# Kernel optimization log

Hardware: AMD Instinct MI355X
Metric: run time of the kernel (lower is better)

## Reference

```python
import jax, jax.numpy as jnp
import numpy as np

DIM = 16      # must equal K*K per the module's reshape structure
K = 4         # kernel_size
HEADS = 8
SCALE = (DIM // HEADS) ** (-0.5)


def setup_inputs() -> dict:
    key = jax.random.key(0)
    k1, k2 = jax.random.split(key)
    x = jax.random.normal(k1, (2, 64, 67, 67), dtype=jnp.float32)
    # torch Linear(dim, 3*dim, bias=False) weight: [3*dim, dim]
    w_qkv = jax.random.normal(k2, (3 * DIM, DIM), dtype=jnp.float32) * 0.1
    return {"x": x, "w_qkv": w_qkv}


def reference(x, w_qkv):
    B, C, H, W = x.shape
    k = K
    Ho, Wo = H - k + 1, W - k + 1          # unfold output grid (stride=1)
    L = Ho * Wo
    # Unfold: patches[b, c, i*k+j, ph, pw] = x[b, c, ph+i, pw+j]
    # (matches torch F.unfold channel ordering c-major, then i, then j)
    patches = jnp.stack(
        [x[:, :, i:i + Ho, j:j + Wo] for i in range(k) for j in range(k)],
        axis=2,
    )  # [B, C, k*k, Ho, Wo]
    seq = L // (k * k)                      # L must be divisible by k*k
    # [B*C*k*k, seq, k*k] -- flatten (Ho,Wo)->L row-major then split into (seq, k*k)
    xu = patches.reshape(B * C * k * k, seq, k * k)
    # tiny attention over each row; feature dim = k*k = DIM
    qkv = xu @ w_qkv.T                      # [N, seq, 3*DIM]
    q, kk_, v = jnp.split(qkv, 3, axis=-1)
    scores = jnp.einsum('nqd,nkd->nqk', q, kk_) * SCALE   # [N, seq, seq]
    attn = jax.nn.softmax(scores, axis=-1)                # dropout = identity (eval)
    ao = jnp.einsum('nqk,nkd->nqd', attn, v)              # [N, seq, DIM]
    ao = ao.reshape(B, C, k, k, Ho, Wo)
    # overlap-add fold back onto the HxW grid
    out = jnp.zeros_like(x)
    for i in range(k):
        for j in range(k):
            out = out.at[:, :, i:Ho + i, j:Wo + j].add(ao[:, :, i, j])
    return out
```

## Files before the change

### kernel.cpp

```cpp
#include <hip/hip_runtime.h>


#define BATCH 2
#define CHAN 64
#define HWDIM 67
#define SEQ 256
#define DIM 16
#define NSEQ 2048
#define PLANE 4096
#define OUT_TOTAL (BATCH * CHAN * HWDIM * HWDIM)
#define ATT_SCALE 0.70710678118654752f
#define LOG2E 1.44269504088896340736f
#define HTILES 17

typedef _Float16 half4 __attribute__((ext_vector_type(4)));
typedef _Float16 half8 __attribute__((ext_vector_type(8)));
typedef float float4v __attribute__((ext_vector_type(4)));
typedef __fp16 fp16x2 __attribute__((ext_vector_type(2)));
typedef unsigned int uint2v __attribute__((ext_vector_type(2)));

static __device__ __forceinline__ half4 mk_half4(float a, float b, float c, float d) {
    fp16x2 lo = __builtin_amdgcn_cvt_pkrtz(a, b);
    fp16x2 hi = __builtin_amdgcn_cvt_pkrtz(c, d);
    uint2v u;
    u[0] = __builtin_bit_cast(unsigned int, lo);
    u[1] = __builtin_bit_cast(unsigned int, hi);
    return __builtin_bit_cast(half4, u);
}

static __device__ __forceinline__ half4 pack4(float4v c) {
    return mk_half4(c[0], c[1], c[2], c[3]);
}

__global__ __launch_bounds__(512, 4) void ska_attn_pass1(
    const float* __restrict__ x,
    const float* __restrict__ w,
    _Float16* __restrict__ ao)
{
    __shared__ __align__(16) _Float16 buf[2][16][64][8];

    const int half_id = threadIdx.x >> 8;
    const int n  = blockIdx.x * 2 + half_id;
    const int p  = n & 15;
    const int bc = n >> 4;
    const int oi = p >> 2;
    const int oj = p & 3;

    const int s   = threadIdx.x & 255;
    const int ph  = s >> 2;
    const int pw0 = (s & 3) * DIM;

    const float* xrow = x + ((size_t)bc * HWDIM + (ph + oi)) * HWDIM + pw0 + oj;
    const int kt = s >> 4, kk = s & 15;
#pragma unroll
    for (int dh = 0; dh < 4; ++dh) {
        const half4 h = mk_half4(xrow[4 * dh + 0], xrow[4 * dh + 1],
                                 xrow[4 * dh + 2], xrow[4 * dh + 3]);
        *(half4*)&buf[half_id][kt][kk + 16 * dh][0] = h;
    }

    const int wave = (threadIdx.x >> 6) & 3;
    const int lane = threadIdx.x & 63;
    const int o = lane & 15;
    const int g = lane >> 4;

    const float4 wq4 = *(const float4*)(w + ( 0 + o) * DIM + 4 * g);
    const float4 wk4 = *(const float4*)(w + (16 + o) * DIM + 4 * g);
    const float4 wv4 = *(const float4*)(w + (32 + o) * DIM + 4 * g);
    const half4 wqf = mk_half4(wq4.x * (ATT_SCALE * LOG2E), wq4.y * (ATT_SCALE * LOG2E),
                               wq4.z * (ATT_SCALE * LOG2E), wq4.w * (ATT_SCALE * LOG2E));
    const half4 wkf = mk_half4(wk4.x, wk4.y, wk4.z, wk4.w);
    const half4 wvf = mk_half4(wv4.x, wv4.y, wv4.z, wv4.w);

    const float4v zf = (float4v){0.f, 0.f, 0.f, 0.f};

    half4 qfr[4];
#pragma unroll
    for (int u = 0; u < 4; ++u) {
        const int t = 4 * wave + u;
        const half4 xf = *(const half4*)&buf[half_id][t][lane][0];
        const half4 kf = pack4(__builtin_amdgcn_mfma_f32_16x16x16f16(wkf, xf, zf, 0, 0, 0));
        const half4 vf = pack4(__builtin_amdgcn_mfma_f32_16x16x16f16(xf, wvf, zf, 0, 0, 0));
        const half8 kv = __builtin_shufflevector(kf, vf, 0, 1, 2, 3, 4, 5, 6, 7);
        *(half8*)&buf[half_id][t][lane][0] = kv;
        qfr[u] = pack4(__builtin_amdgcn_mfma_f32_16x16x16f16(wqf, xf, zf, 0, 0, 0));
    }
    __syncthreads();

    float4v oacc[4];
    float lpart[4];
#pragma unroll
    for (int j = 0; j < 4; ++j) {
        oacc[j] = zf;
        lpart[j] = 0.f;
    }

#pragma unroll 4
    for (int t = 0; t < 16; ++t) {
        const half8 kv = *(const half8*)&buf[half_id][t][lane][0];
        const half4 kf = __builtin_shufflevector(kv, kv, 0, 1, 2, 3);
        const half4 vf = __builtin_shufflevector(kv, kv, 4, 5, 6, 7);
#pragma unroll
        for (int j = 0; j < 4; ++j) {
            float4v sfr = __builtin_amdgcn_mfma_f32_16x16x16f16(kf, qfr[j], zf, 0, 0, 0);
            const float p0 = __builtin_amdgcn_exp2f(sfr[0]);
            const float p1 = __builtin_amdgcn_exp2f(sfr[1]);
            const float p2 = __builtin_amdgcn_exp2f(sfr[2]);
            const float p3 = __builtin_amdgcn_exp2f(sfr[3]);
            lpart[j] += (p0 + p1) + (p2 + p3);
            const half4 pb = mk_half4(p0, p1, p2, p3);
            oacc[j] = __builtin_amdgcn_mfma_f32_16x16x16f16(vf, pb, oacc[j], 0, 0, 0);
        }
    }

#pragma unroll
    for (int j = 0; j < 4; ++j) {
        float lj = lpart[j];
        lj += __shfl_xor(lj, 16, 64);
        lj += __shfl_xor(lj, 32, 64);
        const float rl = 1.f / lj;
        const int query = (4 * wave + j) * 16 + (lane & 15);
        const half4 hv = mk_half4(oacc[j][0] * rl, oacc[j][1] * rl,
                                  oacc[j][2] * rl, oacc[j][3] * rl);
        *(half4*)(ao + (size_t)n * PLANE + query * DIM + 4 * g) = hv;
    }
}

__global__ __launch_bounds__(256) void ska_fold_pass2(
    const _Float16* __restrict__ ao,
    float* __restrict__ out)
{
    __shared__ __align__(16) _Float16 sA[16][4][64];

    const int blk = blockIdx.x;
    const int h0  = (blk % HTILES) * 4;
    const int bc  = blk / HTILES;
    const int tid = threadIdx.x;

    {
        const int pl = tid >> 4;
        const int hh = (tid >> 2) & 3;
        const int pw = (tid & 3) * 16;
        const int i  = pl >> 2;
        const int prow = h0 + hh - i;
        half8 v0, v1;
        if (prow >= 0 && prow < 64) {
            const _Float16* src = ao + ((size_t)(bc * 16 + pl)) * PLANE + prow * 64 + pw;
            v0 = *(const half8*)src;
            v1 = *(const half8*)(src + 8);
        } else {
            const half8 z = (half8)(_Float16)0.f;
            v0 = z; v1 = z;
        }
        *(half8*)&sA[pl][hh][pw]     = v0;
        *(half8*)&sA[pl][hh][pw + 8] = v1;
    }
    __syncthreads();

    for (int px = tid; px < 4 * HWDIM; px += 256) {
        const int hh = px / HWDIM;
        const int ww = px % HWDIM;
        const int h  = h0 + hh;
        if (h >= HWDIM) continue;
        float acc = 0.f;
#pragma unroll
        for (int i = 0; i < 4; ++i) {
#pragma unroll
            for (int j = 0; j < 4; ++j) {
                const int pw = ww - j;
                if (pw < 0 || pw >= 64) continue;
                acc += (float)sA[i * 4 + j][hh][pw];
            }
        }
        out[((size_t)bc * HWDIM + h) * HWDIM + ww] = acc;
    }
}

__global__ __launch_bounds__(256) void ska_attn_atomic(
    const float* __restrict__ x, const float* __restrict__ w,
    float* __restrict__ out)
{
    __shared__ float sw[3 * DIM * DIM];
    __shared__ float sk[SEQ][DIM];
    __shared__ float sv[SEQ][DIM];

    const int n = blockIdx.x, p = n & 15, bc = n >> 4, oi = p >> 2, oj = p & 3;
    const int s = threadIdx.x, ph = s >> 2, pw0 = (s & 3) * DIM;

#pragma unroll
    for (int r = 0; r < 3; ++r) sw[r * 256 + s] = w[r * 256 + s];

    const float* xrow = x + ((size_t)bc * HWDIM + (ph + oi)) * HWDIM + pw0 + oj;
    float xr[DIM];
#pragma unroll
    for (int d = 0; d < DIM; ++d) xr[d] = xrow[d];
    __syncthreads();

    float q[DIM];
#pragma unroll
    for (int o = 0; o < DIM; ++o) {
        float aq = 0.f, ak = 0.f, av = 0.f;
#pragma unroll
        for (int d = 0; d < DIM; ++d) {
            aq += xr[d] * sw[o * DIM + d];
            ak += xr[d] * sw[(DIM + o) * DIM + d];
            av += xr[d] * sw[(2 * DIM + o) * DIM + d];
        }
        q[o] = aq * ATT_SCALE; sk[s][o] = ak; sv[s][o] = av;
    }
    __syncthreads();

    float l = 0.f, acc[DIM];
#pragma unroll
    for (int d = 0; d < DIM; ++d) acc[d] = 0.f;
    for (int t = 0; t < SEQ; ++t) {
        float sc = 0.f;
#pragma unroll
        for (int d = 0; d < DIM; ++d) sc += q[d] * sk[t][d];
        const float pe = __expf(sc);
        l += pe;
#pragma unroll
        for (int d = 0; d < DIM; ++d) acc[d] += pe * sv[t][d];
    }
    const float rl = 1.f / l;
    float* obase = out + ((size_t)bc * HWDIM + (ph + oi)) * HWDIM + pw0 + oj;
#pragma unroll
    for (int d = 0; d < DIM; ++d) atomicAdd(&obase[d], acc[d] * rl);
}

extern "C" void kernel_launch(void* const* d_in, const int* in_sizes, int n_in,
                              void* d_out, int out_size, void* d_ws, size_t ws_size,
                              hipStream_t stream) {
    const float* x = (const float*)d_in[0];
    const float* w = (const float*)d_in[1];
    float* out = (float*)d_out;

    const size_t need = (size_t)NSEQ * PLANE * sizeof(_Float16);
    if (ws_size >= need) {
        _Float16* ao = (_Float16*)d_ws;
        ska_attn_pass1<<<NSEQ / 2, 512, 0, stream>>>(x, w, ao);
        ska_fold_pass2<<<BATCH * CHAN * HTILES, 256, 0, stream>>>(ao, out);
    } else {
        (void)hipMemsetAsync(out, 0, (size_t)out_size * sizeof(float), stream);
        ska_attn_atomic<<<NSEQ, 256, 0, stream>>>(x, w, out);
    }
}
```

Measured before the change: 85.87 us.

## Remap blocks across XCDs, prefetch K/V fragments, raise occupancy bound

Both kernels remap blockIdx so that consecutive logical blocks are spread round-robin over the 8 XCDs. The goal is to keep related sequences and fold tiles together in each XCD's L2. The attention loop now issues all four score MFMAs before the exp/accumulate steps and prefetches the next K/V fragment from LDS one step ahead. The launch-bounds minimum-blocks hint goes from 4 to 6, and the exact reciprocal is replaced by the hardware rcp. These changes risk register pressure or spills under the tighter bound, and rcp slightly reduces normalization precision.

```diff
diff --git a/kernel.cpp b/kernel.cpp
--- a/kernel.cpp
+++ b/kernel.cpp
@@ -32,15 +32,28 @@
     return mk_half4(c[0], c[1], c[2], c[3]);
 }
 
-__global__ __launch_bounds__(512, 4) void ska_attn_pass1(
+static __device__ __forceinline__ void att_step(const half4 vf, const float4v sfr,
+                                                float& l, float4v& oacc) {
+    const float p0 = __builtin_amdgcn_exp2f(sfr[0]);
+    const float p1 = __builtin_amdgcn_exp2f(sfr[1]);
+    const float p2 = __builtin_amdgcn_exp2f(sfr[2]);
+    const float p3 = __builtin_amdgcn_exp2f(sfr[3]);
+    l += (p0 + p1) + (p2 + p3);
+    const half4 pb = mk_half4(p0, p1, p2, p3);
+    oacc = __builtin_amdgcn_mfma_f32_16x16x16f16(vf, pb, oacc, 0, 0, 0);
+}
+
+__global__ __launch_bounds__(512, 6) void ska_attn_pass1(
     const float* __restrict__ x,
     const float* __restrict__ w,
     _Float16* __restrict__ ao)
 {
     __shared__ __align__(16) _Float16 buf[2][16][64][8];
 
+    const int bid = (int)(blockIdx.x & 7) * 128 + (int)(blockIdx.x >> 3);
+
     const int half_id = threadIdx.x >> 8;
-    const int n  = blockIdx.x * 2 + half_id;
+    const int n  = bid * 2 + half_id;
     const int p  = n & 15;
     const int bc = n >> 4;
     const int oi = p >> 2;
@@ -87,41 +100,37 @@
     }
     __syncthreads();
 
-    float4v oacc[4];
-    float lpart[4];
+    float4v oacc0 = zf, oacc1 = zf, oacc2 = zf, oacc3 = zf;
+    float l0 = 0.f, l1 = 0.f, l2 = 0.f, l3 = 0.f;
+
+    half8 kvc = *(const half8*)&buf[half_id][0][lane][0];
+#pragma unroll 2
+    for (int t = 0; t < 16; ++t) {
+        const half8 kvn = *(const half8*)&buf[half_id][(t + 1) & 15][lane][0];
+        const half4 kf = __builtin_shufflevector(kvc, kvc, 0, 1, 2, 3);
+        const half4 vf = __builtin_shufflevector(kvc, kvc, 4, 5, 6, 7);
+        const float4v s0 = __builtin_amdgcn_mfma_f32_16x16x16f16(kf, qfr[0], zf, 0, 0, 0);
+        const float4v s1 = __builtin_amdgcn_mfma_f32_16x16x16f16(kf, qfr[1], zf, 0, 0, 0);
+        const float4v s2 = __builtin_amdgcn_mfma_f32_16x16x16f16(kf, qfr[2], zf, 0, 0, 0);
+        const float4v s3 = __builtin_amdgcn_mfma_f32_16x16x16f16(kf, qfr[3], zf, 0, 0, 0);
+        att_step(vf, s0, l0, oacc0);
+        att_step(vf, s1, l1, oacc1);
+        att_step(vf, s2, l2, oacc2);
+        att_step(vf, s3, l3, oacc3);
+        kvc = kvn;
+    }
+
+    float lp[4] = {l0, l1, l2, l3};
+    float4v oa[4] = {oacc0, oacc1, oacc2, oacc3};
 #pragma unroll
     for (int j = 0; j < 4; ++j) {
-        oacc[j] = zf;
-        lpart[j] = 0.f;
-    }
-
-#pragma unroll 4
-    for (int t = 0; t < 16; ++t) {
-        const half8 kv = *(const half8*)&buf[half_id][t][lane][0];
-        const half4 kf = __builtin_shufflevector(kv, kv, 0, 1, 2, 3);
-        const half4 vf = __builtin_shufflevector(kv, kv, 4, 5, 6, 7);
-#pragma unroll
-        for (int j = 0; j < 4; ++j) {
-            float4v sfr = __builtin_amdgcn_mfma_f32_16x16x16f16(kf, qfr[j], zf, 0, 0, 0);
-            const float p0 = __builtin_amdgcn_exp2f(sfr[0]);
-            const float p1 = __builtin_amdgcn_exp2f(sfr[1]);
-            const float p2 = __builtin_amdgcn_exp2f(sfr[2]);
-            const float p3 = __builtin_amdgcn_exp2f(sfr[3]);
-            lpart[j] += (p0 + p1) + (p2 + p3);
-            const half4 pb = mk_half4(p0, p1, p2, p3);
-            oacc[j] = __builtin_amdgcn_mfma_f32_16x16x16f16(vf, pb, oacc[j], 0, 0, 0);
-        }
-    }
-
-#pragma unroll
-    for (int j = 0; j < 4; ++j) {
-        float lj = lpart[j];
+        float lj = lp[j];
         lj += __shfl_xor(lj, 16, 64);
         lj += __shfl_xor(lj, 32, 64);
-        const float rl = 1.f / lj;
+        const float rl = __builtin_amdgcn_rcpf(lj);
         const int query = (4 * wave + j) * 16 + (lane & 15);
-        const half4 hv = mk_half4(oacc[j][0] * rl, oacc[j][1] * rl,
-                                  oacc[j][2] * rl, oacc[j][3] * rl);
+        const half4 hv = mk_half4(oa[j][0] * rl, oa[j][1] * rl,
+                                  oa[j][2] * rl, oa[j][3] * rl);
         *(half4*)(ao + (size_t)n * PLANE + query * DIM + 4 * g) = hv;
     }
 }
@@ -132,7 +141,7 @@
 {
     __shared__ __align__(16) _Float16 sA[16][4][64];
 
-    const int blk = blockIdx.x;
+    const int blk = (int)(blockIdx.x & 7) * 272 + (int)(blockIdx.x >> 3);
     const int h0  = (blk % HTILES) * 4;
     const int bc  = blk / HTILES;
     const int tid = threadIdx.x;
```

Result: slower. 90.55 us (+5.5%).
